# Performance work log

Hardware: AMD Instinct MI355X
Metric: run time of the kernel (lower is better)

## Reference

```python
import jax, jax.numpy as jnp
import numpy as np

NOPE, ROPE, LORA, VDIM = 128, 64, 512, 128
T, H, S = 1024, 16, 8192
NUM_CHUNKS = 4  # prefix chunks merged via online-softmax LSE combine
SCALING = (NOPE + ROPE) ** -0.5


def setup_inputs() -> dict:
    key = jax.random.key(0)
    k1, k2, k3, k4 = jax.random.split(key, 4)
    q = jax.random.normal(k1, (T, H, NOPE + ROPE), dtype=jnp.float32)
    kv_cache = jax.random.normal(k2, (S, LORA + ROPE), dtype=jnp.float32)  # latent KV cache [S, 576]
    w_kc = jax.random.normal(k3, (H, NOPE, LORA), dtype=jnp.float32) * (NOPE ** -0.5)
    w_vc = jax.random.normal(k4, (H, LORA, VDIM), dtype=jnp.float32) * (LORA ** -0.5)
    return {"q": q, "kv_cache": kv_cache, "w_kc": w_kc, "w_vc": w_vc}


def _chunk_attn(q_full, kv):
    # q_full: [T,H,576], kv chunk: [C,576] (MQA: single latent KV head)
    scores = jnp.einsum('thd,sd->ths', q_full, kv) * SCALING
    lse = jax.nn.logsumexp(scores, axis=-1)               # [T,H]
    p = jnp.exp(scores - lse[..., None])                  # [T,H,C]
    out = jnp.einsum('ths,sl->thl', p, kv[:, :LORA])      # value = latent kv_lora part
    return out, lse


def reference(q, kv_cache, w_kc, w_vc):
    # --- weight-absorbed query projection (forward_absorb) ---
    q_nope, q_pe = q[..., :NOPE], q[..., NOPE:]
    q_lora = jnp.einsum('thn,hnl->thl', q_nope, w_kc)     # bmm(q_nope^T, w_kc)
    q_full = jnp.concatenate([q_lora, q_pe], axis=-1)     # [T,H,576]

    # --- chunked MQA over latent cache with LSE merge (merge_state_v2) ---
    chunks = kv_cache.reshape(NUM_CHUNKS, S // NUM_CHUNKS, LORA + ROPE)
    acc_out, acc_lse = _chunk_attn(q_full, chunks[0])

    def merge(carry, kv):
        a_out, a_lse = carry
        o, lse = _chunk_attn(q_full, kv)
        new_lse = jnp.logaddexp(a_lse, lse)
        new_out = (a_out * jnp.exp(a_lse - new_lse)[..., None]
                   + o * jnp.exp(lse - new_lse)[..., None])
        return (new_out, new_lse), None

    (attn_out, _), _ = jax.lax.scan(merge, (acc_out, acc_lse), chunks[1:])

    # --- weight-absorbed value projection: bmm(attn^T, w_vc) ---
    out = jnp.einsum('thl,hlv->thv', attn_out, w_vc)      # [T,H,128]
    return out.reshape(T, H * VDIM)
```

## Files before the change

kernel.cpp:

```cpp
#include <hip/hip_runtime.h>
#include <stdint.h>
#include <stddef.h>

#define T_TOK 1024
#define NH    16
#define S_KV  8192
#define DQK   576
#define DV    512
#define NROWS (T_TOK*NH)
#define SCALING 0.072168783648703220563f
#define M_FIX 8.0f

#define SC 32
#define NT (S_KV/SC)
#define KV_CH (72*SC)
#define VT_CH (4*DV)

typedef __attribute__((ext_vector_type(8))) short bf16x8;
typedef __attribute__((ext_vector_type(4))) float f32x4;

__device__ __forceinline__ uint16_t f2bf(float f) {
  uint32_t u = __float_as_uint(f);
  u += 0x7FFFu + ((u >> 16) & 1u);
  return (uint16_t)(u >> 16);
}
__device__ __forceinline__ uint32_t pk2(float a, float b) {
  return (uint32_t)f2bf(a) | ((uint32_t)f2bf(b) << 16);
}
__device__ __forceinline__ void async16(void* lds, const void* g) {
  __builtin_amdgcn_global_load_lds((const __attribute__((address_space(1))) void*)g,
                                   (__attribute__((address_space(3))) void*)lds, 16, 0, 0);
}

__global__ void prep_qfull(const float* __restrict__ q, const float* __restrict__ w_kc,
                           uint16_t* __restrict__ q_full) {
  const int h = blockIdx.y, t0 = blockIdx.x * 32;
  const int tid = threadIdx.x;
  __shared__ float qn[32][128];
  #pragma unroll
  for (int r = 0; r < 4; ++r) {
    int idx4 = r * 256 + tid;
    int row = idx4 >> 5, c4 = (idx4 & 31) * 4;
    const float4 v = *(const float4*)(q + ((size_t)((t0 + row) * NH + h)) * 192 + c4);
    *(float4*)&qn[row][c4] = v;
  }
  __syncthreads();
  const int ty = tid >> 6, tx = tid & 63;
  float acc[8][8];
  #pragma unroll
  for (int i = 0; i < 8; ++i)
    #pragma unroll
    for (int j = 0; j < 8; ++j) acc[i][j] = 0.f;
  for (int n = 0; n < 128; ++n) {
    const float4 b0 = *(const float4*)(w_kc + ((size_t)(h * 128 + n)) * 512 + tx * 8);
    const float4 b1 = *(const float4*)(w_kc + ((size_t)(h * 128 + n)) * 512 + tx * 8 + 4);
    #pragma unroll
    for (int i = 0; i < 8; ++i) {
      const float a = qn[ty * 8 + i][n];
      acc[i][0] += a * b0.x; acc[i][1] += a * b0.y; acc[i][2] += a * b0.z; acc[i][3] += a * b0.w;
      acc[i][4] += a * b1.x; acc[i][5] += a * b1.y; acc[i][6] += a * b1.z; acc[i][7] += a * b1.w;
    }
  }
  #pragma unroll
  for (int i = 0; i < 8; ++i) {
    const size_t R = (size_t)(t0 + ty * 8 + i) * NH + h;
    uint4 o;
    o.x = pk2(acc[i][0]*SCALING, acc[i][1]*SCALING);
    o.y = pk2(acc[i][2]*SCALING, acc[i][3]*SCALING);
    o.z = pk2(acc[i][4]*SCALING, acc[i][5]*SCALING);
    o.w = pk2(acc[i][6]*SCALING, acc[i][7]*SCALING);
    *(uint4*)&q_full[R * DQK + tx * 8] = o;
  }
  {
    const int trow = tid >> 3, j0 = (tid & 7) * 8;
    const float* src = q + ((size_t)((t0 + trow) * NH + h)) * 192 + 128 + j0;
    const float4 a = *(const float4*)(src);
    const float4 b = *(const float4*)(src + 4);
    const size_t R = (size_t)(t0 + trow) * NH + h;
    uint4 o;
    o.x = pk2(a.x*SCALING, a.y*SCALING); o.y = pk2(a.z*SCALING, a.w*SCALING);
    o.z = pk2(b.x*SCALING, b.y*SCALING); o.w = pk2(b.z*SCALING, b.w*SCALING);
    *(uint4*)&q_full[R * DQK + 512 + j0] = o;
  }
}

__global__ void prep_kv(const float* __restrict__ kv, uint16_t* __restrict__ kv_t,
                        uint16_t* __restrict__ vt_t) {
  const int st = blockIdx.x, tid = threadIdx.x;
  uint16_t* kvo = kv_t + (size_t)st * (KV_CH * 8);
  #pragma unroll
  for (int r = 0; r < 9; ++r) {
    const int k = r * 256 + tid;
    const int dc = k >> 5, sl = k & 31;
    const float* src = kv + ((size_t)(st * SC + sl)) * DQK + dc * 8;
    const float4 a = *(const float4*)src;
    const float4 b = *(const float4*)(src + 4);
    uint4 o;
    o.x = pk2(a.x, a.y); o.y = pk2(a.z, a.w); o.z = pk2(b.x, b.y); o.w = pk2(b.z, b.w);
    *(uint4*)&kvo[(size_t)k * 8] = o;
  }
  uint16_t* vto = vt_t + (size_t)st * (VT_CH * 8);
  #pragma unroll
  for (int r = 0; r < 8; ++r) {
    const int k = r * 256 + tid;
    const int sc = k >> 9, v = k & 511;
    float val[8];
    #pragma unroll
    for (int e = 0; e < 8; ++e)
      val[e] = kv[((size_t)(st * SC + sc * 8 + e)) * DQK + v];
    uint4 o;
    o.x = pk2(val[0], val[1]); o.y = pk2(val[2], val[3]);
    o.z = pk2(val[4], val[5]); o.w = pk2(val[6], val[7]);
    *(uint4*)&vto[(size_t)k * 8] = o;
  }
}

__global__ void wvt_prep(const float* __restrict__ w_vc, uint16_t* __restrict__ wvt) {
  const int c = blockIdx.x * 256 + threadIdx.x;
  const int h = c >> 13, rem = c & 8191;
  const int lc = rem >> 7, v = rem & 127;
  const float* src = w_vc + ((size_t)h * 512 + lc * 8) * 128 + v;
  float val[8];
  #pragma unroll
  for (int e = 0; e < 8; ++e) val[e] = src[e * 128];
  uint4 o;
  o.x = pk2(val[0], val[1]); o.y = pk2(val[2], val[3]);
  o.z = pk2(val[4], val[5]); o.w = pk2(val[6], val[7]);
  *(uint4*)&wvt[(size_t)c * 8] = o;
}

__global__ __launch_bounds__(768, 3) void attn_kernel(
    const uint16_t* __restrict__ q_full, const uint16_t* __restrict__ kv_t,
    const uint16_t* __restrict__ vt_t, uint16_t* __restrict__ attn_o) {
  __shared__ short kv_lds[2][KV_CH * 8];
  __shared__ short P_lds[2][260 * 8];
  __shared__ float l_sh[64];

  const int tid = threadIdx.x;
  const int wv = tid >> 6, lane = tid & 63;
  const int cc = lane & 15, quad = lane >> 4;
  const int R0 = blockIdx.x * 64;

  if (wv < 4) {
    const int qh = wv;
    bf16x8 qf[18];
    {
      const uint16_t* qrow = q_full + (size_t)(R0 + 16 * qh + cc) * DQK + quad * 8;
      #pragma unroll
      for (int kk = 0; kk < 18; ++kk)
        qf[kk] = *(const bf16x8*)(qrow + kk * 32);
    }
    const int e = cc & 7, scb = cc >> 3;
    const int qb0 = 16 * qh + quad * 4;

    for (int st = 0; st <= NT; ++st) {
      __syncthreads();
      if (st < NT) {
        const short* kb = kv_lds[st & 1];
        f32x4 sa0 = {0.f,0.f,0.f,0.f}, sa1 = {0.f,0.f,0.f,0.f};
        __builtin_amdgcn_s_setprio(1);
        #pragma unroll
        for (int kk = 0; kk < 18; ++kk) {
          const bf16x8 b0 = *(const bf16x8*)&kb[((kk * 4 + quad) * SC + cc) * 8];
          const bf16x8 b1 = *(const bf16x8*)&kb[((kk * 4 + quad) * SC + 16 + cc) * 8];
          sa0 = __builtin_amdgcn_mfma_f32_16x16x32_bf16(qf[kk], b0, sa0, 0, 0, 0);
          sa1 = __builtin_amdgcn_mfma_f32_16x16x32_bf16(qf[kk], b1, sa1, 0, 0, 0);
        }
        __builtin_amdgcn_s_setprio(0);
        short* Pb = P_lds[st & 1];
        #pragma unroll
        for (int r = 0; r < 4; ++r) {
          Pb[(scb * 65 + qb0 + r) * 8 + e]       = (short)f2bf(__expf(sa0[r] - M_FIX));
          Pb[((2 + scb) * 65 + qb0 + r) * 8 + e] = (short)f2bf(__expf(sa1[r] - M_FIX));
        }
      }
    }
    __syncthreads();
  } else {
    const int ci = wv - 4;
    f32x4 acc[4][4];
    #pragma unroll
    for (int a = 0; a < 4; ++a)
      #pragma unroll
      for (int b = 0; b < 4; ++b) acc[a][b] = (f32x4){0.f, 0.f, 0.f, 0.f};
    f32x4 accl[4];
    #pragma unroll
    for (int a = 0; a < 4; ++a) accl[a] = (f32x4){0.f, 0.f, 0.f, 0.f};
    bf16x8 ones;
    #pragma unroll
    for (int e2 = 0; e2 < 8; ++e2) ones[e2] = (short)0x3F80;

    {
      const uint16_t* kt = kv_t;
      #pragma unroll
      for (int r = 0; r < 5; ++r) {
        const int base = r * 512 + ci * 64;
        if (base < KV_CH)
          async16(&kv_lds[0][base * 8], kt + (size_t)(base + lane) * 8);
      }
    }

    for (int st = 0; st <= NT; ++st) {
      __syncthreads();
      bf16x8 vt4[4];
      if (st > 0) {
        const uint16_t* vtile = vt_t + (size_t)(st - 1) * (VT_CH * 8);
        #pragma unroll
        for (int vj = 0; vj < 4; ++vj)
          vt4[vj] = *(const bf16x8*)(vtile + (size_t)(quad * 512 + 64 * ci + 16 * vj + cc) * 8);
      }
      if (st + 1 < NT) {
        const uint16_t* kt = kv_t + (size_t)(st + 1) * (KV_CH * 8);
        short* dst = kv_lds[(st + 1) & 1];
        #pragma unroll
        for (int r = 0; r < 5; ++r) {
          const int base = r * 512 + ci * 64;
          if (base < KV_CH)
            async16(&dst[base * 8], kt + (size_t)(base + lane) * 8);
        }
      }
      if (st > 0) {
        const short* Pb = P_lds[(st - 1) & 1];
        bf16x8 af[4];
        #pragma unroll
        for (int q2 = 0; q2 < 4; ++q2)
          af[q2] = *(const bf16x8*)&Pb[(quad * 65 + 16 * q2 + cc) * 8];
        __builtin_amdgcn_s_setprio(1);
        if (ci == 0) {
          #pragma unroll
          for (int q2 = 0; q2 < 4; ++q2)
            accl[q2] = __builtin_amdgcn_mfma_f32_16x16x32_bf16(af[q2], ones, accl[q2], 0, 0, 0);
        }
        #pragma unroll
        for (int q2 = 0; q2 < 4; ++q2)
          #pragma unroll
          for (int vj = 0; vj < 4; ++vj)
            acc[q2][vj] = __builtin_amdgcn_mfma_f32_16x16x32_bf16(af[q2], vt4[vj], acc[q2][vj], 0, 0, 0);
        __builtin_amdgcn_s_setprio(0);
      }
    }
    if (ci == 0 && cc == 0) {
      #pragma unroll
      for (int q2 = 0; q2 < 4; ++q2)
        #pragma unroll
        for (int r = 0; r < 4; ++r)
          l_sh[16 * q2 + quad * 4 + r] = accl[q2][r];
    }
    __syncthreads();
    #pragma unroll
    for (int q2 = 0; q2 < 4; ++q2) {
      #pragma unroll
      for (int r = 0; r < 4; ++r) {
        const int row = 16 * q2 + quad * 4 + r;
        const float li = 1.0f / l_sh[row];
        #pragma unroll
        for (int vj = 0; vj < 4; ++vj)
          attn_o[(size_t)(R0 + row) * DV + 64 * ci + 16 * vj + cc] = f2bf(acc[q2][vj][r] * li);
      }
    }
  }
}

__global__ __launch_bounds__(256) void out_proj(const uint16_t* __restrict__ attn_o,
                                                const uint16_t* __restrict__ wvt,
                                                float* __restrict__ out) {
  const int h = blockIdx.y, t0 = blockIdx.x * 64;
  const int wv = threadIdx.x >> 6, lane = threadIdx.x & 63;
  const int cc = lane & 15, quad = lane >> 4;

  f32x4 acc[8];
  #pragma unroll
  for (int vj = 0; vj < 8; ++vj) acc[vj] = (f32x4){0.f, 0.f, 0.f, 0.f};

  const uint16_t* arow = attn_o + ((size_t)(t0 + wv * 16 + cc) * NH + h) * DV + quad * 8;
  const uint16_t* wb = wvt + (size_t)h * (64 * 128) * 8;
  #pragma unroll 4
  for (int kk = 0; kk < 16; ++kk) {
    const bf16x8 a = *(const bf16x8*)(arow + kk * 32);
    #pragma unroll
    for (int vj = 0; vj < 8; ++vj) {
      const bf16x8 b = *(const bf16x8*)(wb + (size_t)(((kk * 4 + quad) * 128) + 16 * vj + cc) * 8);
      acc[vj] = __builtin_amdgcn_mfma_f32_16x16x32_bf16(a, b, acc[vj], 0, 0, 0);
    }
  }
  #pragma unroll
  for (int vj = 0; vj < 8; ++vj)
    #pragma unroll
    for (int r = 0; r < 4; ++r)
      out[(size_t)(t0 + wv * 16 + quad * 4 + r) * (NH * 128) + h * 128 + 16 * vj + cc] = acc[vj][r];
}

extern "C" void kernel_launch(void* const* d_in, const int* in_sizes, int n_in,
                              void* d_out, int out_size, void* d_ws, size_t ws_size,
                              hipStream_t stream) {
  const float* q    = (const float*)d_in[0];
  const float* kv   = (const float*)d_in[1];
  const float* w_kc = (const float*)d_in[2];
  const float* w_vc = (const float*)d_in[3];
  float* out = (float*)d_out;

  char* ws = (char*)d_ws;
  const size_t SZ_QF = (size_t)NROWS * DQK * 2;
  const size_t SZ_KT = (size_t)NT * KV_CH * 16;
  const size_t SZ_VT = (size_t)NT * VT_CH * 16;
  const size_t SZ_AO = (size_t)NROWS * DV * 2;
  uint16_t* q_full = (uint16_t*)(ws);
  uint16_t* kv_t   = (uint16_t*)(ws + SZ_QF);
  uint16_t* vt_t   = (uint16_t*)(ws + SZ_QF + SZ_KT);
  uint16_t* attn_o = (uint16_t*)(ws + SZ_QF + SZ_KT + SZ_VT);
  uint16_t* wvt    = (uint16_t*)(ws + SZ_QF + SZ_KT + SZ_VT + SZ_AO);

  prep_qfull<<<dim3(32, 16), 256, 0, stream>>>(q, w_kc, q_full);
  prep_kv<<<NT, 256, 0, stream>>>(kv, kv_t, vt_t);
  wvt_prep<<<512, 256, 0, stream>>>(w_vc, wvt);
  attn_kernel<<<256, 768, 0, stream>>>(q_full, kv_t, vt_t, attn_o);
  out_proj<<<dim3(16, 16), 256, 0, stream>>>(attn_o, wvt, out);
}
```

Measured before the change: 413.4 us.

## Defer softmax exp by one stage and fold log2e into query scale

```diff
diff --git a/kernel.cpp b/kernel.cpp
--- a/kernel.cpp
+++ b/kernel.cpp
@@ -8,8 +8,8 @@
 #define DQK   576
 #define DV    512
 #define NROWS (T_TOK*NH)
-#define SCALING 0.072168783648703220563f
-#define M_FIX 8.0f
+#define SCALE2 0.104117546f
+#define M_FIX2 11.5415603f
 
 #define SC 32
 #define NT (S_KV/SC)
@@ -65,10 +65,10 @@
   for (int i = 0; i < 8; ++i) {
     const size_t R = (size_t)(t0 + ty * 8 + i) * NH + h;
     uint4 o;
-    o.x = pk2(acc[i][0]*SCALING, acc[i][1]*SCALING);
-    o.y = pk2(acc[i][2]*SCALING, acc[i][3]*SCALING);
-    o.z = pk2(acc[i][4]*SCALING, acc[i][5]*SCALING);
-    o.w = pk2(acc[i][6]*SCALING, acc[i][7]*SCALING);
+    o.x = pk2(acc[i][0]*SCALE2, acc[i][1]*SCALE2);
+    o.y = pk2(acc[i][2]*SCALE2, acc[i][3]*SCALE2);
+    o.z = pk2(acc[i][4]*SCALE2, acc[i][5]*SCALE2);
+    o.w = pk2(acc[i][6]*SCALE2, acc[i][7]*SCALE2);
     *(uint4*)&q_full[R * DQK + tx * 8] = o;
   }
   {
@@ -78,8 +78,8 @@
     const float4 b = *(const float4*)(src + 4);
     const size_t R = (size_t)(t0 + trow) * NH + h;
     uint4 o;
-    o.x = pk2(a.x*SCALING, a.y*SCALING); o.y = pk2(a.z*SCALING, a.w*SCALING);
-    o.z = pk2(b.x*SCALING, b.y*SCALING); o.w = pk2(b.z*SCALING, b.w*SCALING);
+    o.x = pk2(a.x*SCALE2, a.y*SCALE2); o.y = pk2(a.z*SCALE2, a.w*SCALE2);
+    o.z = pk2(b.x*SCALE2, b.y*SCALE2); o.w = pk2(b.z*SCALE2, b.w*SCALE2);
     *(uint4*)&q_full[R * DQK + 512 + j0] = o;
   }
 }
@@ -153,11 +153,23 @@
     const int e = cc & 7, scb = cc >> 3;
     const int qb0 = 16 * qh + quad * 4;
 
-    for (int st = 0; st <= NT; ++st) {
+    f32x4 sa0 = {0.f,0.f,0.f,0.f}, sa1 = {0.f,0.f,0.f,0.f};
+    for (int st = 0; st <= NT + 1; ++st) {
       __syncthreads();
+      if (st >= 1 && st <= NT) {
+        short* Pb = P_lds[(st - 1) & 1];
+        #pragma unroll
+        for (int r = 0; r < 4; ++r) {
+          float p0, p1;
+          asm("v_exp_f32 %0, %1" : "=v"(p0) : "v"(sa0[r] - M_FIX2));
+          asm("v_exp_f32 %0, %1" : "=v"(p1) : "v"(sa1[r] - M_FIX2));
+          Pb[(scb * 65 + qb0 + r) * 8 + e]       = (short)f2bf(p0);
+          Pb[((2 + scb) * 65 + qb0 + r) * 8 + e] = (short)f2bf(p1);
+        }
+      }
       if (st < NT) {
         const short* kb = kv_lds[st & 1];
-        f32x4 sa0 = {0.f,0.f,0.f,0.f}, sa1 = {0.f,0.f,0.f,0.f};
+        sa0 = (f32x4){0.f,0.f,0.f,0.f}; sa1 = (f32x4){0.f,0.f,0.f,0.f};
         __builtin_amdgcn_s_setprio(1);
         #pragma unroll
         for (int kk = 0; kk < 18; ++kk) {
@@ -167,12 +179,6 @@
           sa1 = __builtin_amdgcn_mfma_f32_16x16x32_bf16(qf[kk], b1, sa1, 0, 0, 0);
         }
         __builtin_amdgcn_s_setprio(0);
-        short* Pb = P_lds[st & 1];
-        #pragma unroll
-        for (int r = 0; r < 4; ++r) {
-          Pb[(scb * 65 + qb0 + r) * 8 + e]       = (short)f2bf(__expf(sa0[r] - M_FIX));
-          Pb[((2 + scb) * 65 + qb0 + r) * 8 + e] = (short)f2bf(__expf(sa1[r] - M_FIX));
-        }
       }
     }
     __syncthreads();
@@ -200,11 +206,11 @@
       }
     }
 
-    for (int st = 0; st <= NT; ++st) {
+    for (int st = 0; st <= NT + 1; ++st) {
       __syncthreads();
       bf16x8 vt4[4];
-      if (st > 0) {
-        const uint16_t* vtile = vt_t + (size_t)(st - 1) * (VT_CH * 8);
+      if (st >= 2) {
+        const uint16_t* vtile = vt_t + (size_t)(st - 2) * (VT_CH * 8);
         #pragma unroll
         for (int vj = 0; vj < 4; ++vj)
           vt4[vj] = *(const bf16x8*)(vtile + (size_t)(quad * 512 + 64 * ci + 16 * vj + cc) * 8);
@@ -219,8 +225,8 @@
             async16(&dst[base * 8], kt + (size_t)(base + lane) * 8);
         }
       }
-      if (st > 0) {
-        const short* Pb = P_lds[(st - 1) & 1];
+      if (st >= 2) {
+        const short* Pb = P_lds[(st - 2) & 1];
         bf16x8 af[4];
         #pragma unroll
         for (int q2 = 0; q2 < 4; ++q2)
```

After: 424.5 us. +2.7%, slower.
